# Kernel optimization log

Hardware: AMD Instinct MI355X
Metric: run time of the kernel (lower is better)

## Reference

```python
import jax, jax.numpy as jnp
import numpy as np

N = 100000   # nodes
E = 1600000  # edges
IN = 128
HID = 128
OUT = 40
EPS = 1e-5


def setup_inputs() -> dict:
    key = jax.random.key(0)
    ks = jax.random.split(key, 8)
    x = jax.random.normal(ks[0], (N, IN), jnp.float32)
    edge_index = jax.random.randint(ks[1], (2, E), 0, N, dtype=jnp.int32)
    W1 = jax.random.normal(ks[2], (IN, HID), jnp.float32) / np.float32(np.sqrt(IN))
    b1 = jnp.zeros((HID,), jnp.float32)
    g1 = jnp.ones((HID,), jnp.float32)
    be1 = jnp.zeros((HID,), jnp.float32)
    W2 = jax.random.normal(ks[3], (HID, HID), jnp.float32) / np.float32(np.sqrt(HID))
    b2 = jnp.zeros((HID,), jnp.float32)
    g2 = jnp.ones((HID,), jnp.float32)
    be2 = jnp.zeros((HID,), jnp.float32)
    W3 = jax.random.normal(ks[4], (HID, OUT), jnp.float32) / np.float32(np.sqrt(HID))
    b3 = jnp.zeros((OUT,), jnp.float32)
    return dict(x=x, edge_index=edge_index, W1=W1, b1=b1, g1=g1, be1=be1,
                W2=W2, b2=b2, g2=g2, be2=be2, W3=W3, b3=b3)


def _gcn_norm(edge_index, n):
    # PyG gcn_norm: add self loops, symmetric D^-1/2 (A+I) D^-1/2 weights
    loop = jnp.arange(n, dtype=edge_index.dtype)
    src = jnp.concatenate([edge_index[0], loop])
    dst = jnp.concatenate([edge_index[1], loop])
    deg = jax.ops.segment_sum(jnp.ones_like(dst, jnp.float32), dst, num_segments=n)
    dinv = jnp.where(deg > 0, jax.lax.rsqrt(deg), 0.0)
    norm = dinv[src] * dinv[dst]  # [E+N]
    return src, dst, norm


def _gcn_conv(x, W, b, src, dst, norm, n):
    h = x @ W                                   # [N, F]
    msg = h[src] * norm[:, None]                # gather + scale  [E+N, F]
    agg = jax.ops.segment_sum(msg, dst, num_segments=n)
    return agg + b


def _batchnorm(x, g, be):
    mu = jnp.mean(x, axis=0)
    var = jnp.var(x, axis=0)
    return (x - mu) * jax.lax.rsqrt(var + EPS) * g + be


def reference(x, edge_index, W1, b1, g1, be1, W2, b2, g2, be2, W3, b3):
    n = x.shape[0]
    src, dst, norm = _gcn_norm(edge_index, n)
    h = _gcn_conv(x, W1, b1, src, dst, norm, n)
    h = jax.nn.relu(_batchnorm(h, g1, be1))
    h = _gcn_conv(h, W2, b2, src, dst, norm, n)
    h = jax.nn.relu(_batchnorm(h, g2, be2))
    h = _gcn_conv(h, W3, b3, src, dst, norm, n)
    return jax.nn.softmax(h, axis=-1)
```

## Files before the change

### kernel.cpp

```cpp
#include <hip/hip_runtime.h>
#include <hip/hip_fp16.h>

#define NN   100000
#define NE   1600000
#define NBUCK 391
#define NW1   512
#define CH1   (NE / NW1)
#define GN    (NBUCK * NW1)
#define SC    512
#define SNB   (GN / SC)
#define BNB   512
constexpr float EPSV = 1e-5f;

typedef _Float16 f16x8 __attribute__((ext_vector_type(8)));
typedef float    f32x4 __attribute__((ext_vector_type(4)));


__global__ __launch_bounds__(256) void p1hist_kernel(const int* __restrict__ dst,
                                                     int* __restrict__ G) {
    __shared__ int h[NBUCK];
    int t = threadIdx.x, wg = blockIdx.x;
    for (int i = t; i < NBUCK; i += 256) h[i] = 0;
    __syncthreads();
    int base = wg * CH1;
    for (int e = base + t; e < base + CH1; e += 256)
        atomicAdd(&h[dst[e] >> 8], 1);
    __syncthreads();
    for (int i = t; i < NBUCK; i += 256) G[i * NW1 + wg] = h[i];
}

__global__ __launch_bounds__(256) void gscan1_kernel(const int* __restrict__ G,
                                                     int* __restrict__ bsum) {
    __shared__ int red[256];
    int t = threadIdx.x;
    int base = blockIdx.x * SC + t * 2;
    red[t] = G[base] + G[base + 1];
    __syncthreads();
    #pragma unroll
    for (int off = 128; off > 0; off >>= 1) {
        if (t < off) red[t] += red[t + off];
        __syncthreads();
    }
    if (t == 0) bsum[blockIdx.x] = red[0];
}

__global__ __launch_bounds__(512) void gscan2_kernel(const int* __restrict__ bsum,
                                                     int* __restrict__ boff) {
    __shared__ int s[512];
    int t = threadIdx.x;
    int v = (t < SNB) ? bsum[t] : 0;
    s[t] = v;
    __syncthreads();
    #pragma unroll
    for (int off = 1; off < 512; off <<= 1) {
        int u = (t >= off) ? s[t - off] : 0;
        __syncthreads();
        s[t] += u;
        __syncthreads();
    }
    if (t < SNB) boff[t] = s[t] - v;
}

__global__ __launch_bounds__(256) void gscan3_kernel(int* __restrict__ G,
                                                     const int* __restrict__ boff) {
    __shared__ int s[256];
    int t = threadIdx.x;
    int base = blockIdx.x * SC + t * 2;
    int c0 = G[base], c1 = G[base + 1];
    int pair = c0 + c1;
    s[t] = pair;
    __syncthreads();
    #pragma unroll
    for (int off = 1; off < 256; off <<= 1) {
        int u = (t >= off) ? s[t - off] : 0;
        __syncthreads();
        s[t] += u;
        __syncthreads();
    }
    int excl = boff[blockIdx.x] + s[t] - pair;
    G[base]     = excl;
    G[base + 1] = excl + c0;
}

__global__ __launch_bounds__(256) void p1fill_kernel(const int* __restrict__ src,
                                                     const int* __restrict__ dst,
                                                     const int* __restrict__ G,
                                                     int* __restrict__ ebuf) {
    __shared__ int cur[NBUCK];
    int t = threadIdx.x, wg = blockIdx.x;
    for (int i = t; i < NBUCK; i += 256) cur[i] = G[i * NW1 + wg];
    __syncthreads();
    int base = wg * CH1;
    for (int e = base + t; e < base + CH1; e += 256) {
        int d = dst[e];
        int pos = atomicAdd(&cur[d >> 8], 1);
        ebuf[pos] = src[e] | ((d & 255) << 17);
    }
}

__global__ __launch_bounds__(256) void p2build_kernel(const int* __restrict__ ebuf,
                                                      const int* __restrict__ G,
                                                      int* __restrict__ rowptr,
                                                      int* __restrict__ srcsorted,
                                                      float* __restrict__ dinv) {
    __shared__ int cnt[256];
    __shared__ int s[256];
    __shared__ int cur[256];
    int t = threadIdx.x, b = blockIdx.x;
    int base = G[b * NW1];
    int endp = (b == NBUCK - 1) ? NE : G[(b + 1) * NW1];
    cnt[t] = 0;
    __syncthreads();
    for (int e = base + t; e < endp; e += 256)
        atomicAdd(&cnt[ebuf[e] >> 17], 1);
    __syncthreads();
    int c = cnt[t];
    s[t] = c;
    __syncthreads();
    #pragma unroll
    for (int off = 1; off < 256; off <<= 1) {
        int u = (t >= off) ? s[t - off] : 0;
        __syncthreads();
        s[t] += u;
        __syncthreads();
    }
    int excl = s[t] - c;
    int node = b * 256 + t;
    if (node < NN) {
        rowptr[node] = base + excl;
        dinv[node]   = rsqrtf((float)c + 1.0f);
    }
    cur[t] = base + excl;
    __syncthreads();
    for (int e = base + t; e < endp; e += 256) {
        int p = ebuf[e];
        int pos = atomicAdd(&cur[p >> 17], 1);
        srcsorted[pos] = p & 0x1FFFF;
    }
    if (b == NBUCK - 1 && t == 0) rowptr[NN] = NE;
}


__global__ void wprep_kernel(const float* __restrict__ W1, const float* __restrict__ W2,
                             __half* __restrict__ Wt) {
    int b = blockIdx.x;
    int layer = b >> 7, n = b & 127, k = threadIdx.x;
    const float* W = layer ? W2 : W1;
    Wt[layer * 16384 + n * 128 + k] = __float2half_rn(W[k * 128 + n]);
}


__global__ __launch_bounds__(256) void bnstats_kernel(const __half* __restrict__ X,
                                                      float* __restrict__ partial) {
    __shared__ float red[4][256];
    int t = threadIdx.x;
    int f2 = t & 63, rg = t >> 6;
    const __half2* base = (const __half2*)X + f2;
    float s0 = 0.f, s1 = 0.f, q0 = 0.f, q1 = 0.f;
    for (int r = blockIdx.x * 4 + rg; r < NN; r += BNB * 4) {
        float2 v = __half22float2(base[(size_t)r * 64]);
        s0 += v.x; s1 += v.y; q0 += v.x * v.x; q1 += v.y * v.y;
    }
    red[rg][f2 * 4 + 0] = s0;
    red[rg][f2 * 4 + 1] = s1;
    red[rg][f2 * 4 + 2] = q0;
    red[rg][f2 * 4 + 3] = q1;
    __syncthreads();
    int kind = t >> 7, f = t & 127;
    int slot = (f >> 1) * 4 + (f & 1) + kind * 2;
    float v = red[0][slot] + red[1][slot] + red[2][slot] + red[3][slot];
    partial[blockIdx.x * 256 + kind * 128 + f] = v;
}

__global__ __launch_bounds__(256) void bnfinal_kernel(const float* __restrict__ partial,
                                                      const float* __restrict__ g,
                                                      const float* __restrict__ be,
                                                      float* __restrict__ sc) {
    __shared__ float red[256];
    int t = threadIdx.x;
    float v = 0.f;
    #pragma unroll 8
    for (int sl = 0; sl < BNB; ++sl) v += partial[sl * 256 + t];
    red[t] = v;
    __syncthreads();
    if (t < 128) {
        float s = red[t], q = red[128 + t];
        float mu  = s * (1.0f / NN);
        float var = q * (1.0f / NN) - mu * mu;
        float rstd = rsqrtf(var + EPSV);
        float scale = g[t] * rstd;
        sc[t]       = scale;
        sc[128 + t] = be[t] - mu * scale;
    }
}


__device__ __forceinline__ int swzb(int row, int colByte) {
    return row * 256 + (colByte ^ ((row & 7) << 4));
}

template<bool BN, typename TIN>
__global__ __launch_bounds__(256) void gemm128m_kernel(const TIN* __restrict__ X,
        const __half* __restrict__ Wt, const float* __restrict__ sc,
        const float* __restrict__ dinv, __half* __restrict__ Y) {
    __shared__ __align__(16) char Xs[64 * 256];
    __shared__ __align__(16) char Wts[128 * 256];
    __shared__ float dvs[64];
    int tid = threadIdx.x;
    int node0 = blockIdx.x * 64;

    {
        int n = tid >> 1, c0 = (tid & 1) * 64;
        const _Float16* g = (const _Float16*)Wt + n * 128 + c0;
        #pragma unroll
        for (int j = 0; j < 8; ++j) {
            f16x8 v = *(const f16x8*)(g + j * 8);
            *(f16x8*)(Wts + swzb(n, (c0 + j * 8) * 2)) = v;
        }
    }
    {
        int r = tid >> 2, c0 = (tid & 3) * 32;
        int grow = node0 + r;
        #pragma unroll
        for (int j = 0; j < 4; ++j) {
            int c = c0 + j * 8;
            f16x8 o;
            if (grow < NN) {
                float f[8];
                if constexpr (sizeof(TIN) == 4) {
                    float4 u0 = *(const float4*)((const float*)X + (size_t)grow * 128 + c);
                    float4 u1 = *(const float4*)((const float*)X + (size_t)grow * 128 + c + 4);
                    f[0] = u0.x; f[1] = u0.y; f[2] = u0.z; f[3] = u0.w;
                    f[4] = u1.x; f[5] = u1.y; f[6] = u1.z; f[7] = u1.w;
                } else {
                    f16x8 h = *(const f16x8*)((const _Float16*)X + (size_t)grow * 128 + c);
                    #pragma unroll
                    for (int i = 0; i < 8; ++i) f[i] = (float)h[i];
                }
                #pragma unroll
                for (int i = 0; i < 8; ++i) {
                    if constexpr (BN) f[i] = fmaxf(fmaf(f[i], sc[c + i], sc[128 + c + i]), 0.f);
                    o[i] = (_Float16)f[i];
                }
            } else {
                #pragma unroll
                for (int i = 0; i < 8; ++i) o[i] = (_Float16)0.f;
            }
            *(f16x8*)(Xs + swzb(r, c * 2)) = o;
        }
    }
    if (tid < 64) dvs[tid] = (node0 + tid < NN) ? dinv[node0 + tid] : 0.f;
    __syncthreads();

    int lane = tid & 63;
    int wv   = tid >> 6;
    int n0w  = wv * 32;
    int lm   = lane & 15;
    int lg   = lane >> 4;

    f32x4 acc[4][2] = {};
    #pragma unroll
    for (int s = 0; s < 4; ++s) {
        int kb = (s * 32 + lg * 8) * 2;
        f16x8 a[4], b[2];
        #pragma unroll
        for (int i = 0; i < 4; ++i)
            a[i] = *(const f16x8*)(Xs + swzb(i * 16 + lm, kb));
        #pragma unroll
        for (int r = 0; r < 2; ++r)
            b[r] = *(const f16x8*)(Wts + swzb(n0w + r * 16 + lm, kb));
        #pragma unroll
        for (int i = 0; i < 4; ++i)
            #pragma unroll
            for (int r = 0; r < 2; ++r)
                acc[i][r] = __builtin_amdgcn_mfma_f32_16x16x32_f16(a[i], b[r], acc[i][r], 0, 0, 0);
    }

    _Float16* Yh = (_Float16*)Y;
    #pragma unroll
    for (int i = 0; i < 4; ++i) {
        #pragma unroll
        for (int q = 0; q < 4; ++q) {
            int row = i * 16 + lg * 4 + q;
            int grow = node0 + row;
            if (grow < NN) {
                float di = dvs[row];
                Yh[(size_t)grow * 128 + n0w + lm]      = (_Float16)(acc[i][0][q] * di);
                Yh[(size_t)grow * 128 + n0w + 16 + lm] = (_Float16)(acc[i][1][q] * di);
            }
        }
    }
}


__global__ __launch_bounds__(256) void gemm40_kernel(const __half* __restrict__ X,
        const float* __restrict__ W, const float* __restrict__ sc,
        const float* __restrict__ dinv, __half* __restrict__ Y) {
    __shared__ float Ws[128][40];
    __shared__ float Xs[32][132];
    int tx = threadIdx.x, ty = threadIdx.y;
    int tid = ty * 8 + tx;
    int node0 = blockIdx.x * 32;

    float* wf = &Ws[0][0];
    for (int idx = tid; idx < 128 * 40; idx += 256) wf[idx] = W[idx];
    for (int idx = tid * 8; idx < 32 * 128; idx += 256 * 8) {
        int n = idx >> 7, f = idx & 127;
        f16x8 h = *(const f16x8*)((const _Float16*)X + (size_t)(node0 + n) * 128 + f);
        float v[8];
        #pragma unroll
        for (int i = 0; i < 8; ++i)
            v[i] = fmaxf(fmaf((float)h[i], sc[f + i], sc[128 + f + i]), 0.f);
        *(float4*)&Xs[n][f]     = make_float4(v[0], v[1], v[2], v[3]);
        *(float4*)&Xs[n][f + 4] = make_float4(v[4], v[5], v[6], v[7]);
    }
    __syncthreads();

    float acc[5] = {0, 0, 0, 0, 0};
    int f0 = tx * 5;
    #pragma unroll 4
    for (int k = 0; k < 128; ++k) {
        float xv = Xs[ty][k];
        #pragma unroll
        for (int j = 0; j < 5; ++j) acc[j] = fmaf(xv, Ws[k][f0 + j], acc[j]);
    }
    float di = dinv[node0 + ty];
    __half* yp = Y + (size_t)(node0 + ty) * 40 + f0;
    #pragma unroll
    for (int j = 0; j < 5; ++j) yp[j] = __float2half_rn(acc[j] * di);
}


__global__ __launch_bounds__(256) void agg128_kernel(const __half* __restrict__ H,
        const int* __restrict__ rowptr, const int* __restrict__ srcs,
        const float* __restrict__ dinv, const float* __restrict__ bias,
        __half* __restrict__ Bout) {
    int wave = threadIdx.x >> 6;
    int lane = threadIdx.x & 63;
    int node = blockIdx.x * 4 + wave;
    int beg = rowptr[node], end = rowptr[node + 1];
    int c = lane * 2;
    float a0 = 0.f, a1 = 0.f, b0 = 0.f, b1 = 0.f;
    int e = beg;
    for (; e + 3 < end; e += 4) {
        int s0 = srcs[e], s1 = srcs[e + 1], s2 = srcs[e + 2], s3 = srcs[e + 3];
        float2 f0 = __half22float2(*(const __half2*)(H + (size_t)s0 * 128 + c));
        float2 f1 = __half22float2(*(const __half2*)(H + (size_t)s1 * 128 + c));
        float2 f2 = __half22float2(*(const __half2*)(H + (size_t)s2 * 128 + c));
        float2 f3 = __half22float2(*(const __half2*)(H + (size_t)s3 * 128 + c));
        a0 += f0.x + f1.x; a1 += f0.y + f1.y;
        b0 += f2.x + f3.x; b1 += f2.y + f3.y;
    }
    for (; e < end; ++e) {
        int s = srcs[e];
        float2 f = __half22float2(*(const __half2*)(H + (size_t)s * 128 + c));
        a0 += f.x; a1 += f.y;
    }
    float di = dinv[node];
    float2 hs = __half22float2(*(const __half2*)(H + (size_t)node * 128 + c));
    a0 = di * (a0 + b0 + hs.x) + bias[c];
    a1 = di * (a1 + b1 + hs.y) + bias[c + 1];
    __half2 hv;
    hv.x = __float2half_rn(a0); hv.y = __float2half_rn(a1);
    *(__half2*)(Bout + (size_t)node * 128 + c) = hv;
}

__global__ __launch_bounds__(256) void agg40_softmax_kernel(const __half* __restrict__ H,
        const int* __restrict__ rowptr, const int* __restrict__ srcs,
        const float* __restrict__ dinv, const float* __restrict__ bias,
        float* __restrict__ out) {
    int wave = threadIdx.x >> 6;
    int lane = threadIdx.x & 63;
    int node = blockIdx.x * 4 + wave;
    int beg = rowptr[node], end = rowptr[node + 1];
    bool act = lane < 40;
    int ln = act ? lane : 0;
    float a0 = 0.f, a1 = 0.f, a2 = 0.f, a3 = 0.f;
    int e = beg;
    for (; e + 3 < end; e += 4) {
        int s0 = srcs[e], s1 = srcs[e + 1], s2 = srcs[e + 2], s3 = srcs[e + 3];
        a0 += __half2float(H[(size_t)s0 * 40 + ln]);
        a1 += __half2float(H[(size_t)s1 * 40 + ln]);
        a2 += __half2float(H[(size_t)s2 * 40 + ln]);
        a3 += __half2float(H[(size_t)s3 * 40 + ln]);
    }
    for (; e < end; ++e) a0 += __half2float(H[(size_t)srcs[e] * 40 + ln]);
    float di = dinv[node];
    float hs = __half2float(H[(size_t)node * 40 + ln]);
    float v = act ? (di * (a0 + a1 + a2 + a3 + hs) + bias[ln]) : -3.0e38f;
    float m = v;
    #pragma unroll
    for (int off = 32; off > 0; off >>= 1) m = fmaxf(m, __shfl_xor(m, off));
    float ev = act ? expf(v - m) : 0.f;
    float ssum = ev;
    #pragma unroll
    for (int off = 32; off > 0; off >>= 1) ssum += __shfl_xor(ssum, off);
    if (act) out[(size_t)node * 40 + lane] = ev / ssum;
}


extern "C" void kernel_launch(void* const* d_in, const int* in_sizes, int n_in,
                              void* d_out, int out_size, void* d_ws, size_t ws_size,
                              hipStream_t stream) {
    const float* x   = (const float*)d_in[0];
    const int*   ei  = (const int*)d_in[1];
    const float* W1  = (const float*)d_in[2];
    const float* b1  = (const float*)d_in[3];
    const float* g1  = (const float*)d_in[4];
    const float* be1 = (const float*)d_in[5];
    const float* W2  = (const float*)d_in[6];
    const float* b2  = (const float*)d_in[7];
    const float* g2  = (const float*)d_in[8];
    const float* be2 = (const float*)d_in[9];
    const float* W3  = (const float*)d_in[10];
    const float* b3  = (const float*)d_in[11];
    float* out = (float*)d_out;
    const int* src = ei;
    const int* dst = ei + NE;

    char* p = (char*)d_ws;
    auto alloc = [&](size_t bytes) { char* r = p; p += (bytes + 255) & ~255ull; return r; };
    int*    rowptr    = (int*)   alloc((size_t)(NN + 1) * 4);
    int*    srcsorted = (int*)   alloc((size_t)NE * 4);
    float*  dinv      = (float*) alloc((size_t)NN * 4);
    float*  sc        = (float*) alloc(256 * 4);
    int*    G         = (int*)   alloc((size_t)GN * 4);
    int*    bsum      = (int*)   alloc((size_t)SNB * 4);
    int*    boff      = (int*)   alloc((size_t)SNB * 4);
    float*  partial   = (float*) alloc((size_t)BNB * 256 * 4);
    __half* Wth       = (__half*)alloc((size_t)2 * 16384 * 2);
    __half* A         = (__half*)alloc((size_t)NN * 128 * 2);
    __half* Bh        = (__half*)alloc((size_t)NN * 128 * 2);
    int*    ebuf      = (int*)A;

    wprep_kernel<<<256, 128, 0, stream>>>(W1, W2, Wth);
    p1hist_kernel<<<NW1, 256, 0, stream>>>(dst, G);
    gscan1_kernel<<<SNB, 256, 0, stream>>>(G, bsum);
    gscan2_kernel<<<1, 512, 0, stream>>>(bsum, boff);
    gscan3_kernel<<<SNB, 256, 0, stream>>>(G, boff);
    p1fill_kernel<<<NW1, 256, 0, stream>>>(src, dst, G, ebuf);
    p2build_kernel<<<NBUCK, 256, 0, stream>>>(ebuf, G, rowptr, srcsorted, dinv);

    const int GB = (NN + 63) / 64;
    gemm128m_kernel<false, float><<<GB, 256, 0, stream>>>(x, Wth, nullptr, dinv, A);
    agg128_kernel<<<NN / 4, 256, 0, stream>>>(A, rowptr, srcsorted, dinv, b1, Bh);
    bnstats_kernel<<<BNB, 256, 0, stream>>>(Bh, partial);
    bnfinal_kernel<<<1, 256, 0, stream>>>(partial, g1, be1, sc);
    gemm128m_kernel<true, __half><<<GB, 256, 0, stream>>>(Bh, Wth + 16384, sc, dinv, A);
    agg128_kernel<<<NN / 4, 256, 0, stream>>>(A, rowptr, srcsorted, dinv, b2, Bh);
    bnstats_kernel<<<BNB, 256, 0, stream>>>(Bh, partial);
    bnfinal_kernel<<<1, 256, 0, stream>>>(partial, g2, be2, sc);
    gemm40_kernel<<<NN / 32, dim3(8, 32), 0, stream>>>(Bh, W3, sc, dinv, A);
    agg40_softmax_kernel<<<NN / 4, 256, 0, stream>>>(A, rowptr, srcsorted, dinv, b3, out);
}
```

Measured before the change: 434.9 us.

## Vectorize neighbor gathers with 16-byte loads and pad 40-wide features to 64

The 128-wide aggregation now splits each wave into four lane groups. Each group gathers a different edge's row using 16-byte f16x8 loads, and the partial sums are combined with cross-lane shuffles. The last layer's transformed features are stored with a padded row stride of 64 halfs, zero-filled beyond column 40, so the softmax aggregation can also use 16-byte loads with eight edges in flight. The softmax becomes a reduction over lane segments with vectorized float4 output stores. The aim is fewer, wider memory transactions and more gathers in flight per wave. The costs are extra shuffle reductions, the padded buffer needing more workspace, and lanes idling on low-degree nodes.

After: 417.5 us. 4.0% less time.

```diff
diff --git a/kernel.cpp b/kernel.cpp
--- a/kernel.cpp
+++ b/kernel.cpp
@@ -325,9 +325,11 @@
         for (int j = 0; j < 5; ++j) acc[j] = fmaf(xv, Ws[k][f0 + j], acc[j]);
     }
     float di = dinv[node0 + ty];
-    __half* yp = Y + (size_t)(node0 + ty) * 40 + f0;
-    #pragma unroll
-    for (int j = 0; j < 5; ++j) yp[j] = __float2half_rn(acc[j] * di);
+    __half* yp = Y + (size_t)(node0 + ty) * 64;
+    #pragma unroll
+    for (int j = 0; j < 5; ++j) yp[f0 + j] = __float2half_rn(acc[j] * di);
+    #pragma unroll
+    for (int j = 0; j < 3; ++j) yp[40 + tx * 3 + j] = __float2half_rn(0.f);
 }
 
 
@@ -339,30 +341,46 @@
     int lane = threadIdx.x & 63;
     int node = blockIdx.x * 4 + wave;
     int beg = rowptr[node], end = rowptr[node + 1];
-    int c = lane * 2;
-    float a0 = 0.f, a1 = 0.f, b0 = 0.f, b1 = 0.f;
+    int g = lane >> 4;
+    int c = lane & 15;
+    const f16x8* Hc = (const f16x8*)H + c;
+    float acc[8] = {};
     int e = beg;
+    for (; e + 7 < end; e += 8) {
+        int s0 = srcs[e + g];
+        int s1 = srcs[e + 4 + g];
+        f16x8 h0 = Hc[(size_t)s0 * 16];
+        f16x8 h1 = Hc[(size_t)s1 * 16];
+        #pragma unroll
+        for (int j = 0; j < 8; ++j) acc[j] += (float)h0[j] + (float)h1[j];
+    }
     for (; e + 3 < end; e += 4) {
-        int s0 = srcs[e], s1 = srcs[e + 1], s2 = srcs[e + 2], s3 = srcs[e + 3];
-        float2 f0 = __half22float2(*(const __half2*)(H + (size_t)s0 * 128 + c));
-        float2 f1 = __half22float2(*(const __half2*)(H + (size_t)s1 * 128 + c));
-        float2 f2 = __half22float2(*(const __half2*)(H + (size_t)s2 * 128 + c));
-        float2 f3 = __half22float2(*(const __half2*)(H + (size_t)s3 * 128 + c));
-        a0 += f0.x + f1.x; a1 += f0.y + f1.y;
-        b0 += f2.x + f3.x; b1 += f2.y + f3.y;
-    }
-    for (; e < end; ++e) {
-        int s = srcs[e];
-        float2 f = __half22float2(*(const __half2*)(H + (size_t)s * 128 + c));
-        a0 += f.x; a1 += f.y;
+        int s0 = srcs[e + g];
+        f16x8 h0 = Hc[(size_t)s0 * 16];
+        #pragma unroll
+        for (int j = 0; j < 8; ++j) acc[j] += (float)h0[j];
+    }
+    if (e + g < end) {
+        int s = srcs[e + g];
+        f16x8 h = Hc[(size_t)s * 16];
+        #pragma unroll
+        for (int j = 0; j < 8; ++j) acc[j] += (float)h[j];
+    }
+    #pragma unroll
+    for (int j = 0; j < 8; ++j) {
+        acc[j] += __shfl_xor(acc[j], 16);
+        acc[j] += __shfl_xor(acc[j], 32);
     }
     float di = dinv[node];
-    float2 hs = __half22float2(*(const __half2*)(H + (size_t)node * 128 + c));
-    a0 = di * (a0 + b0 + hs.x) + bias[c];
-    a1 = di * (a1 + b1 + hs.y) + bias[c + 1];
-    __half2 hv;
-    hv.x = __float2half_rn(a0); hv.y = __float2half_rn(a1);
-    *(__half2*)(Bout + (size_t)node * 128 + c) = hv;
+    f16x8 hs = Hc[(size_t)node * 16];
+    _Float16 o[8];
+    #pragma unroll
+    for (int j = 0; j < 8; ++j) {
+        float v = di * (acc[j] + (float)hs[j]) + bias[c * 8 + j];
+        o[j] = (_Float16)v;
+    }
+    if (g == 0)
+        *((f16x8*)Bout + (size_t)node * 16 + c) = *(f16x8*)o;
 }
 
 __global__ __launch_bounds__(256) void agg40_softmax_kernel(const __half* __restrict__ H,
@@ -373,29 +391,67 @@
     int lane = threadIdx.x & 63;
     int node = blockIdx.x * 4 + wave;
     int beg = rowptr[node], end = rowptr[node + 1];
-    bool act = lane < 40;
-    int ln = act ? lane : 0;
-    float a0 = 0.f, a1 = 0.f, a2 = 0.f, a3 = 0.f;
+    int g = lane >> 3;
+    int c = lane & 7;
+    const f16x8* Hc = (const f16x8*)H + c;
+    float acc[8] = {};
     int e = beg;
-    for (; e + 3 < end; e += 4) {
-        int s0 = srcs[e], s1 = srcs[e + 1], s2 = srcs[e + 2], s3 = srcs[e + 3];
-        a0 += __half2float(H[(size_t)s0 * 40 + ln]);
-        a1 += __half2float(H[(size_t)s1 * 40 + ln]);
-        a2 += __half2float(H[(size_t)s2 * 40 + ln]);
-        a3 += __half2float(H[(size_t)s3 * 40 + ln]);
-    }
-    for (; e < end; ++e) a0 += __half2float(H[(size_t)srcs[e] * 40 + ln]);
+    for (; e + 15 < end; e += 16) {
+        int s0 = srcs[e + g];
+        int s1 = srcs[e + 8 + g];
+        f16x8 h0 = Hc[(size_t)s0 * 8];
+        f16x8 h1 = Hc[(size_t)s1 * 8];
+        #pragma unroll
+        for (int j = 0; j < 8; ++j) acc[j] += (float)h0[j] + (float)h1[j];
+    }
+    for (; e + 7 < end; e += 8) {
+        int s0 = srcs[e + g];
+        f16x8 h0 = Hc[(size_t)s0 * 8];
+        #pragma unroll
+        for (int j = 0; j < 8; ++j) acc[j] += (float)h0[j];
+    }
+    if (e + g < end) {
+        int s = srcs[e + g];
+        f16x8 h = Hc[(size_t)s * 8];
+        #pragma unroll
+        for (int j = 0; j < 8; ++j) acc[j] += (float)h[j];
+    }
+    #pragma unroll
+    for (int j = 0; j < 8; ++j) {
+        acc[j] += __shfl_xor(acc[j], 8);
+        acc[j] += __shfl_xor(acc[j], 16);
+        acc[j] += __shfl_xor(acc[j], 32);
+    }
     float di = dinv[node];
-    float hs = __half2float(H[(size_t)node * 40 + ln]);
-    float v = act ? (di * (a0 + a1 + a2 + a3 + hs) + bias[ln]) : -3.0e38f;
-    float m = v;
-    #pragma unroll
-    for (int off = 32; off > 0; off >>= 1) m = fmaxf(m, __shfl_xor(m, off));
-    float ev = act ? expf(v - m) : 0.f;
-    float ssum = ev;
-    #pragma unroll
-    for (int off = 32; off > 0; off >>= 1) ssum += __shfl_xor(ssum, off);
-    if (act) out[(size_t)node * 40 + lane] = ev / ssum;
+    f16x8 hs = Hc[(size_t)node * 8];
+    bool real = c < 5;
+    float v[8];
+    float mloc = -3.0e38f;
+    #pragma unroll
+    for (int j = 0; j < 8; ++j) {
+        float b = real ? bias[c * 8 + j] : 0.f;
+        v[j] = di * (acc[j] + (float)hs[j]) + b;
+        if (real) mloc = fmaxf(mloc, v[j]);
+    }
+    mloc = fmaxf(mloc, __shfl_xor(mloc, 1));
+    mloc = fmaxf(mloc, __shfl_xor(mloc, 2));
+    mloc = fmaxf(mloc, __shfl_xor(mloc, 4));
+    float ev[8];
+    float sloc = 0.f;
+    #pragma unroll
+    for (int j = 0; j < 8; ++j) {
+        ev[j] = real ? expf(v[j] - mloc) : 0.f;
+        sloc += ev[j];
+    }
+    sloc += __shfl_xor(sloc, 1);
+    sloc += __shfl_xor(sloc, 2);
+    sloc += __shfl_xor(sloc, 4);
+    float inv = 1.0f / sloc;
+    if (g == 0 && real) {
+        float* op = out + (size_t)node * 40 + c * 8;
+        *(float4*)op       = make_float4(ev[0] * inv, ev[1] * inv, ev[2] * inv, ev[3] * inv);
+        *(float4*)(op + 4) = make_float4(ev[4] * inv, ev[5] * inv, ev[6] * inv, ev[7] * inv);
+    }
 }
 
 
```
